# Kernel optimization log

Measured on AMD Instinct MI355X. Metric: run time of the kernel, lower is better.

The kernel has to match this reference:

```python
import jax, jax.numpy as jnp
import numpy as np
import math

B, T, N, D = 8, 12, 1000, 256
H, R = 8, 32
HD = D // H
E = 4 * D  # SwiGLU expansion


def setup_inputs() -> dict:
    key = jax.random.key(0)
    ks = jax.random.split(key, 12)
    s = 0.02
    return {
        "x": jax.random.normal(ks[0], (B, T, N, D), jnp.float32),
        "z": jax.random.normal(ks[1], (B, T, N, D), jnp.float32),
        # block params
        "norm1_w": jnp.ones((D,), jnp.float32),
        "norm2_w": jnp.ones((D,), jnp.float32),
        "alpha": jnp.float32(math.log(9)),
        "beta": jnp.float32(math.log(math.sqrt(2) + 1)),
        "gamma": jnp.float32(math.log(9)),
        "delta": jnp.float32(math.log(math.sqrt(2) + 1)),
        # low-rank attention params (Linear stored as [in, out])
        "Wq": jax.random.normal(ks[2], (D, D), jnp.float32) * s,
        "bq": jnp.zeros((D,), jnp.float32),
        "key_param": jax.random.normal(ks[3], (R, H, HD), jnp.float32),
        "Wv": jax.random.normal(ks[4], (D, D), jnp.float32) * s,
        "bv": jnp.zeros((D,), jnp.float32),
        "mha_alpha": jnp.full((H, 1), math.log(9), jnp.float32),
        "mha_beta": jnp.full((H, 1), math.log(0.01), jnp.float32),
        # SwiGLU FFN params
        "W1": jax.random.normal(ks[5], (D, E), jnp.float32) * s,
        "b1": jnp.zeros((E,), jnp.float32),
        "W2": jax.random.normal(ks[6], (D, E), jnp.float32) * s,
        "b2": jnp.zeros((E,), jnp.float32),
        "W3": jax.random.normal(ks[7], (E, D), jnp.float32) * s,
        "b3": jnp.zeros((D,), jnp.float32),
    }


def _rms_norm(x, w, eps=1e-6):
    return w * (x * jax.lax.rsqrt(jnp.mean(x * x, axis=-1, keepdims=True) + eps))


def reference(x, z, norm1_w, norm2_w, alpha, beta, gamma, delta,
              Wq, bq, key_param, Wv, bv, mha_alpha, mha_beta,
              W1, b1, W2, b2, W3, b3):
    sig = jax.nn.sigmoid
    x1 = _rms_norm(x, norm1_w)
    z1 = _rms_norm(sig(gamma) * x1 + sig(delta) * z, norm2_w)

    # SwiGLU FFN (dropout is identity in eval)
    ffn = (jax.nn.silu(x1 @ W1 + b1) * (x1 @ W2 + b2)) @ W3 + b3

    # Low-rank spatial attention
    q = (z1 @ Wq + bq).reshape(B, T, N, H, HD)
    attn = jnp.einsum('btnhd,rhd->btnhr', q, key_param) / jnp.float32(HD) ** 0.5
    xv = (x1 @ Wv + bv).reshape(B, T, N, H, HD)
    v = jnp.einsum('btnhr,btnhd->btrhd', jax.nn.softmax(attn, axis=-1), xv)
    v = jnp.einsum('btnhr,btrhd->btnhd', jax.nn.softmax(attn, axis=2), v)
    v = sig(mha_alpha) * xv + sig(mha_beta) * v  # (H,1) broadcasts over (h,d)
    mha = v.reshape(B, T, N, D)

    return sig(alpha) * ffn + sig(beta) * mha
```

## Files before the change

kernel.cpp:

```cpp
#include <hip/hip_runtime.h>
#include <math.h>

#define MT 96000
#define DD 256
#define EE 1024
#define NBT 96
#define NSEQ 1000

typedef __attribute__((ext_vector_type(8))) short bf16x8;
typedef __attribute__((ext_vector_type(4))) short bf16x4;
typedef __attribute__((ext_vector_type(4))) float f32x4;

__device__ __forceinline__ short f2b(float f) {
  union { float f; unsigned u; } v; v.f = f;
  unsigned r = (v.u + 0x7FFFu + ((v.u >> 16) & 1u)) >> 16;
  return (short)r;
}
__device__ __forceinline__ float b2f(short s) {
  union { unsigned u; float f; } v; v.u = ((unsigned)(unsigned short)s) << 16;
  return v.f;
}
__device__ __forceinline__ float sigf(float x) { return 1.f / (1.f + __expf(-x)); }
__device__ __forceinline__ f32x4 mfma16(bf16x8 a, bf16x8 b, f32x4 c) {
  return __builtin_amdgcn_mfma_f32_16x16x32_bf16(a, b, c, 0, 0, 0);
}
__device__ __forceinline__ unsigned cvtpk(float lo, float hi) {
  unsigned r;
  asm("v_cvt_pk_bf16_f32 %0, %1, %2" : "=v"(r) : "v"(lo), "v"(hi));
  return r;
}
__device__ __forceinline__ float frcp(float x) {
  float r;
  asm("v_rcp_f32 %0, %1" : "=v"(r) : "v"(x));
  return r;
}
__device__ __forceinline__ void gl_lds16(const short* gp, short* lp) {
  __builtin_amdgcn_global_load_lds(
      (const __attribute__((address_space(1))) void*)gp,
      (__attribute__((address_space(3))) void*)lp, 16, 0, 0);
}

__global__ __launch_bounds__(256) void k_prep(
    const float* __restrict__ Wq, const float* __restrict__ bq,
    const float* __restrict__ key, const float* __restrict__ Wv,
    const float* __restrict__ W1, const float* __restrict__ W2,
    const float* __restrict__ W3,
    short* __restrict__ W1t, short* __restrict__ W2t, short* __restrict__ W3t,
    short* __restrict__ Wvt, short* __restrict__ Wqkt, float* __restrict__ bqk)
{
  int i = blockIdx.x * 256 + threadIdx.x;
  { int e = i >> 8, c = i & 255;
    W1t[i] = f2b(W1[c * EE + e]);
    W2t[i] = f2b(W2[c * EE + e]); }
  { int n = i >> 10, e = i & 1023;
    W3t[i] = f2b(W3[e * DD + n]); }
  if (i < 65536) {
    int n = i >> 8, c = i & 255;
    Wvt[i] = f2b(Wv[c * DD + n]);
    int h = n >> 5, r = n & 31;
    float acc = 0.f;
    for (int d = 0; d < 32; ++d)
      acc += Wq[c * DD + h * 32 + d] * key[(r * 8 + h) * 32 + d];
    Wqkt[i] = f2b(acc * 0.17677669529663687f);
  }
  if (i < 256) {
    int h = i >> 5, r = i & 31;
    float acc = 0.f;
    for (int d = 0; d < 32; ++d)
      acc += bq[h * 32 + d] * key[(r * 8 + h) * 32 + d];
    bqk[i] = acc * 0.17677669529663687f;
  }
}

__global__ __launch_bounds__(256) void k_norm(
    const float* __restrict__ x, const float* __restrict__ z,
    const float* __restrict__ nw1, const float* __restrict__ nw2,
    const float* __restrict__ gamma, const float* __restrict__ delta,
    short* __restrict__ x1bp, short* __restrict__ z1bp)
{
  int tok = blockIdx.x * 4 + (threadIdx.x >> 6);
  int lane = threadIdx.x & 63;
  size_t rbase = (size_t)tok * DD;
  float4 xv = ((const float4*)(x + rbase))[lane];
  float ss = xv.x*xv.x + xv.y*xv.y + xv.z*xv.z + xv.w*xv.w;
  #pragma unroll
  for (int mm = 1; mm < 64; mm <<= 1) ss += __shfl_xor(ss, mm);
  float inv = rsqrtf(ss * 0.00390625f + 1e-6f);
  float4 wv = ((const float4*)nw1)[lane];
  float xa = xv.x * inv * wv.x, xb = xv.y * inv * wv.y,
        xc = xv.z * inv * wv.z, xd = xv.w * inv * wv.w;
  bf16x4 xo = { f2b(xa), f2b(xb), f2b(xc), f2b(xd) };
  ((bf16x4*)(x1bp + rbase))[lane] = xo;
  float sg = sigf(gamma[0]), sd = sigf(delta[0]);
  float4 zv = ((const float4*)(z + rbase))[lane];
  float t0 = sg*xa + sd*zv.x, t1 = sg*xb + sd*zv.y,
        t2 = sg*xc + sd*zv.z, t3 = sg*xd + sd*zv.w;
  float s2 = t0*t0 + t1*t1 + t2*t2 + t3*t3;
  #pragma unroll
  for (int mm = 1; mm < 64; mm <<= 1) s2 += __shfl_xor(s2, mm);
  float inv2 = rsqrtf(s2 * 0.00390625f + 1e-6f);
  float4 w2v = ((const float4*)nw2)[lane];
  bf16x4 zo = { f2b(t0*inv2*w2v.x), f2b(t1*inv2*w2v.y),
                f2b(t2*inv2*w2v.z), f2b(t3*inv2*w2v.w) };
  ((bf16x4*)(z1bp + rbase))[lane] = zo;
}

__global__ __launch_bounds__(256) void k_gemm_fullN(
    const short* __restrict__ A, const short* __restrict__ Bt,
    const float* __restrict__ bias, short* __restrict__ C)
{
  __shared__ __align__(16) short As[64 * 264];
  int row0 = blockIdx.x * 64;
  int tid = threadIdx.x, lane = tid & 63, w = tid >> 6;
  int l15 = lane & 15, g = lane >> 4;
  #pragma unroll
  for (int it = 0; it < 8; ++it) {
    int idx = it * 256 + tid;
    int rw = idx >> 5, ch = (idx & 31) * 8;
    *(bf16x8*)&As[rw * 264 + ch] = *(const bf16x8*)&A[(size_t)(row0 + rw) * 256 + ch];
  }
  f32x4 acc[4][4];
  #pragma unroll
  for (int tn = 0; tn < 4; ++tn) {
    float bb = bias[w * 64 + tn * 16 + l15];
    #pragma unroll
    for (int tm = 0; tm < 4; ++tm) acc[tm][tn] = (f32x4){bb, bb, bb, bb};
  }
  __syncthreads();
  #pragma unroll
  for (int kk = 0; kk < 8; ++kk) {
    bf16x8 af[4], wf[4];
    #pragma unroll
    for (int tm = 0; tm < 4; ++tm)
      af[tm] = *(const bf16x8*)&As[(tm * 16 + l15) * 264 + kk * 32 + g * 8];
    #pragma unroll
    for (int tn = 0; tn < 4; ++tn)
      wf[tn] = *(const bf16x8*)&Bt[(size_t)(w * 64 + tn * 16 + l15) * 256 + kk * 32 + g * 8];
    #pragma unroll
    for (int tn = 0; tn < 4; ++tn)
      #pragma unroll
      for (int tm = 0; tm < 4; ++tm)
        acc[tm][tn] = mfma16(af[tm], wf[tn], acc[tm][tn]);
  }
  #pragma unroll
  for (int tn = 0; tn < 4; ++tn) {
    int n = w * 64 + tn * 16 + l15;
    #pragma unroll
    for (int tm = 0; tm < 4; ++tm)
      #pragma unroll
      for (int r = 0; r < 4; ++r) {
        int m = row0 + tm * 16 + g * 4 + r;
        C[(size_t)m * 256 + n] = f2b(acc[tm][tn][r]);
      }
  }
}

__global__ __launch_bounds__(256, 2) void k_ffn(
    const short* __restrict__ x1bp,
    const short* __restrict__ W1t, const short* __restrict__ W2t,
    const short* __restrict__ W3t,
    const float* __restrict__ b1, const float* __restrict__ b2,
    const float* __restrict__ b3, const float* __restrict__ alpha,
    float* __restrict__ out)
{
  __shared__ __align__(16) short As[64 * 256];
  __shared__ __align__(16) short Hs[64 * 72];
  __shared__ __align__(16) short WR[4 * 4096];
  __shared__ __align__(16) short Bb[2048];
  int row0 = blockIdx.x * 64;
  int tid = threadIdx.x, lane = tid & 63, w = tid >> 6;
  int l15 = lane & 15, g = lane >> 4;
  int swz = l15 & 7;
  int w16 = w * 16;
  int wb = w * 4096;
  int lr = lane >> 2;
  int lc = (((lane & 3) ^ ((lane >> 3) & 3)) * 8);
  int rsw = (l15 >> 1) & 3;

  #pragma unroll
  for (int it = 0; it < 8; ++it) {
    int idx = it * 256 + tid;
    int rw = idx >> 5, c = idx & 31;
    bf16x8 v = __builtin_nontemporal_load(
        (const bf16x8*)&x1bp[(size_t)(row0 + rw) * 256 + c * 8]);
    *(bf16x8*)&As[rw * 256 + ((c ^ (rw & 7)) * 8)] = v;
  }
  {
    float4 v1 = ((const float4*)b1)[tid];
    float4 v2 = ((const float4*)b2)[tid];
    bf16x4 p1 = { f2b(v1.x), f2b(v1.y), f2b(v1.z), f2b(v1.w) };
    bf16x4 p2 = { f2b(v2.x), f2b(v2.y), f2b(v2.z), f2b(v2.w) };
    *(bf16x4*)&Bb[tid * 4] = p1;
    *(bf16x4*)&Bb[1024 + tid * 4] = p2;
  }
  f32x4 oacc[4][4];
  #pragma unroll
  for (int tn = 0; tn < 4; ++tn) {
    float bb = b3[w * 64 + tn * 16 + l15];
    #pragma unroll
    for (int tm = 0; tm < 4; ++tm) oacc[tm][tn] = (f32x4){bb, bb, bb, bb};
  }
  __syncthreads();

  #pragma unroll
  for (int s = 0; s < 4; ++s) {
    gl_lds16(W1t + (size_t)(w16 + lr) * 256 + s * 32 + lc, &WR[wb + s * 1024]);
    gl_lds16(W2t + (size_t)(w16 + lr) * 256 + s * 32 + lc, &WR[wb + s * 1024 + 512]);
  }

  for (int ec = 0; ec < 16; ++ec) {
    int e0 = ec * 64;
    int e0n = ((ec + 1) & 15) * 64;
    int ew = e0 + w16;
    bf16x4 c1b = *(const bf16x4*)&Bb[ew + g * 4];
    bf16x4 c2b = *(const bf16x4*)&Bb[1024 + ew + g * 4];
    f32x4 i1 = { b2f(c1b[0]), b2f(c1b[1]), b2f(c1b[2]), b2f(c1b[3]) };
    f32x4 i2 = { b2f(c2b[0]), b2f(c2b[1]), b2f(c2b[2]), b2f(c2b[3]) };
    f32x4 h1[4], h2[4];
    #pragma unroll
    for (int tm = 0; tm < 4; ++tm) { h1[tm] = i1; h2[tm] = i2; }
    #pragma unroll
    for (int kk = 0; kk < 8; ++kk) {
      int slot = kk & 3;
      asm volatile("s_waitcnt vmcnt(6)" ::: "memory");
      bf16x8 w1f = *(const bf16x8*)&WR[wb + slot * 1024 + l15 * 32 + ((g ^ rsw) * 8)];
      bf16x8 w2f = *(const bf16x8*)&WR[wb + slot * 1024 + 512 + l15 * 32 + ((g ^ rsw) * 8)];
      int ac = ((kk * 4 + g) ^ swz) * 8;
      bf16x8 a0 = *(const bf16x8*)&As[(l15) * 256 + ac];
      bf16x8 a1 = *(const bf16x8*)&As[(16 + l15) * 256 + ac];
      bf16x8 a2 = *(const bf16x8*)&As[(32 + l15) * 256 + ac];
      bf16x8 a3 = *(const bf16x8*)&As[(48 + l15) * 256 + ac];
      asm volatile("s_waitcnt lgkmcnt(0)" ::: "memory");
      if (kk < 4) {
        gl_lds16(W1t + (size_t)(ew + lr) * 256 + (kk + 4) * 32 + lc,
                 &WR[wb + slot * 1024]);
        gl_lds16(W2t + (size_t)(ew + lr) * 256 + (kk + 4) * 32 + lc,
                 &WR[wb + slot * 1024 + 512]);
      } else {
        int k2i = (kk - 4) >> 1, nh = kk & 1;
        const short* g3 = W3t + (size_t)(w * 64 + nh * 32 + lr) * 1024
                          + e0 + k2i * 32 + lc;
        gl_lds16(g3, &WR[wb + slot * 1024]);
        gl_lds16(g3 + 16 * 1024, &WR[wb + slot * 1024 + 512]);
      }
      h1[0] = mfma16(w1f, a0, h1[0]); h2[0] = mfma16(w2f, a0, h2[0]);
      h1[1] = mfma16(w1f, a1, h1[1]); h2[1] = mfma16(w2f, a1, h2[1]);
      h1[2] = mfma16(w1f, a2, h1[2]); h2[2] = mfma16(w2f, a2, h2[2]);
      h1[3] = mfma16(w1f, a3, h1[3]); h2[3] = mfma16(w2f, a3, h2[3]);
    }
    #pragma unroll
    for (int tm = 0; tm < 4; ++tm) {
      int m = tm * 16 + l15;
      float a0 = h1[tm][0], a1 = h1[tm][1], a2 = h1[tm][2], a3 = h1[tm][3];
      float v0 = a0 * h2[tm][0] * sigf(a0);
      float v1 = a1 * h2[tm][1] * sigf(a1);
      float v2 = a2 * h2[tm][2] * sigf(a2);
      float v3 = a3 * h2[tm][3] * sigf(a3);
      uint2 pk;
      pk.x = cvtpk(v0, v1);
      pk.y = cvtpk(v2, v3);
      *(uint2*)&Hs[m * 72 + w16 + g * 4] = pk;
    }
    asm volatile("s_waitcnt lgkmcnt(0)" ::: "memory");
    __builtin_amdgcn_sched_barrier(0);
    __builtin_amdgcn_s_barrier();
    __builtin_amdgcn_sched_barrier(0);
    #pragma unroll
    for (int k2 = 0; k2 < 2; ++k2) {
      asm volatile("s_waitcnt vmcnt(4)" ::: "memory");
      bf16x8 hf[4];
      #pragma unroll
      for (int tm = 0; tm < 4; ++tm)
        hf[tm] = *(const bf16x8*)&Hs[(tm * 16 + l15) * 72 + k2 * 32 + g * 8];
      bf16x8 w3f[4];
      #pragma unroll
      for (int tn = 0; tn < 4; ++tn)
        w3f[tn] = *(const bf16x8*)&WR[wb + (k2 * 2 + (tn >> 1)) * 1024
                                     + (tn & 1) * 512 + l15 * 32 + ((g ^ rsw) * 8)];
      asm volatile("s_waitcnt lgkmcnt(0)" ::: "memory");
      gl_lds16(W1t + (size_t)(e0n + w16 + lr) * 256 + (k2 * 2) * 32 + lc,
               &WR[wb + (k2 * 2) * 1024]);
      gl_lds16(W2t + (size_t)(e0n + w16 + lr) * 256 + (k2 * 2) * 32 + lc,
               &WR[wb + (k2 * 2) * 1024 + 512]);
      gl_lds16(W1t + (size_t)(e0n + w16 + lr) * 256 + (k2 * 2 + 1) * 32 + lc,
               &WR[wb + (k2 * 2 + 1) * 1024]);
      gl_lds16(W2t + (size_t)(e0n + w16 + lr) * 256 + (k2 * 2 + 1) * 32 + lc,
               &WR[wb + (k2 * 2 + 1) * 1024 + 512]);
      #pragma unroll
      for (int tn = 0; tn < 4; ++tn)
        #pragma unroll
        for (int tm = 0; tm < 4; ++tm)
          oacc[tm][tn] = mfma16(hf[tm], w3f[tn], oacc[tm][tn]);
    }
    __builtin_amdgcn_sched_barrier(0);
    __builtin_amdgcn_s_barrier();
    __builtin_amdgcn_sched_barrier(0);
  }
  asm volatile("s_waitcnt vmcnt(0)" ::: "memory");
  float sa = sigf(alpha[0]);
  #pragma unroll
  for (int tn = 0; tn < 4; ++tn) {
    int n = w * 64 + tn * 16 + l15;
    #pragma unroll
    for (int tm = 0; tm < 4; ++tm)
      #pragma unroll
      for (int r = 0; r < 4; ++r) {
        int m = row0 + tm * 16 + g * 4 + r;
        __builtin_nontemporal_store(sa * oacc[tm][tn][r], &out[(size_t)m * 256 + n]);
      }
  }
}

__global__ __launch_bounds__(256) void k_attn1(
    const short* __restrict__ attnb, const short* __restrict__ xvb,
    float* __restrict__ v1buf, float* __restrict__ colmax, float* __restrict__ colsum)
{
  __shared__ float xr[8][32];
  __shared__ float red[8][32][32];
  __shared__ float mred[8][32], sred[8][32];
  int gid = blockIdx.x;
  int bt = gid >> 3, h = gid & 7;
  int tid = threadIdx.x, r = tid & 31, nl = tid >> 5;
  int base = bt * NSEQ;
  float accd[32];
  #pragma unroll
  for (int d = 0; d < 32; ++d) accd[d] = 0.f;
  float mrun = -1e30f, srun = 0.f;
  for (int it = 0; it < 125; ++it) {
    int tok = base + it * 8 + nl;
    float a = b2f(attnb[(size_t)tok * 256 + h * 32 + r]);
    float rmax = a;
    #pragma unroll
    for (int mm = 16; mm > 0; mm >>= 1) rmax = fmaxf(rmax, __shfl_xor(rmax, mm));
    float ea = __expf(a - rmax);
    float rsum = ea;
    #pragma unroll
    for (int mm = 16; mm > 0; mm >>= 1) rsum += __shfl_xor(rsum, mm);
    float p1 = ea * frcp(rsum);
    float nm = fmaxf(mrun, a);
    srun = srun * __expf(mrun - nm) + __expf(a - nm);
    mrun = nm;
    xr[nl][r] = b2f(xvb[(size_t)tok * 256 + h * 32 + r]);
    #pragma unroll
    for (int d = 0; d < 32; ++d) accd[d] += p1 * xr[nl][d];
  }
  #pragma unroll
  for (int d = 0; d < 32; ++d) red[nl][r][d] = accd[d];
  mred[nl][r] = mrun; sred[nl][r] = srun;
  __syncthreads();
  for (int s = 4; s > 0; s >>= 1) {
    if (nl < s)
      #pragma unroll
      for (int d = 0; d < 32; ++d) red[nl][r][d] += red[nl + s][r][d];
    __syncthreads();
  }
  if (nl == 0) {
    for (int d = 0; d < 32; ++d) v1buf[gid * 1024 + r * 32 + d] = red[0][r][d];
    float Mv = -1e30f;
    for (int j = 0; j < 8; ++j) Mv = fmaxf(Mv, mred[j][r]);
    float Sv = 0.f;
    for (int j = 0; j < 8; ++j) Sv += sred[j][r] * __expf(mred[j][r] - Mv);
    colmax[gid * 32 + r] = Mv;
    colsum[gid * 32 + r] = Sv;
  }
}

__global__ __launch_bounds__(256) void k_attn2(
    const short* __restrict__ attnb, const short* __restrict__ xvb,
    const float* __restrict__ v1buf, const float* __restrict__ colmax,
    const float* __restrict__ colsum, const float* __restrict__ mha_alpha,
    const float* __restrict__ mha_beta, const float* __restrict__ beta,
    float* __restrict__ out)
{
  __shared__ float p2s[256];
  int bt = blockIdx.x, chunk = blockIdx.y;
  int tid = threadIdx.x;
  int h = tid >> 5, d = tid & 31;
  float v1reg[32];
  #pragma unroll
  for (int rr = 0; rr < 32; ++rr)
    v1reg[rr] = v1buf[(size_t)bt * 8192 + h * 1024 + rr * 32 + d];
  float cm  = colmax[bt * 256 + tid];
  float rcs = 1.f / colsum[bt * 256 + tid];
  float sa = sigf(mha_alpha[h]), sb = sigf(mha_beta[h]);
  float sbeta = sigf(beta[0]);
  int tok0 = bt * NSEQ + chunk * 100;
  for (int tl = 0; tl < 100; ++tl) {
    int tok = tok0 + tl;
    float a = b2f(attnb[(size_t)tok * 256 + tid]);
    p2s[tid] = __expf(a - cm) * rcs;
    float xvv = b2f(xvb[(size_t)tok * 256 + tid]);
    float v2 = 0.f;
    #pragma unroll
    for (int rr = 0; rr < 32; ++rr)
      v2 += p2s[h * 32 + rr] * v1reg[rr];
    out[(size_t)tok * 256 + tid] += sbeta * (sa * xvv + sb * v2);
  }
}

extern "C" void kernel_launch(void* const* d_in, const int* in_sizes, int n_in,
                              void* d_out, int out_size, void* d_ws, size_t ws_size,
                              hipStream_t stream) {
  const float* x        = (const float*)d_in[0];
  const float* z        = (const float*)d_in[1];
  const float* norm1_w  = (const float*)d_in[2];
  const float* norm2_w  = (const float*)d_in[3];
  const float* alpha    = (const float*)d_in[4];
  const float* beta     = (const float*)d_in[5];
  const float* gamma    = (const float*)d_in[6];
  const float* delta    = (const float*)d_in[7];
  const float* Wq       = (const float*)d_in[8];
  const float* bq       = (const float*)d_in[9];
  const float* key      = (const float*)d_in[10];
  const float* Wv       = (const float*)d_in[11];
  const float* bv       = (const float*)d_in[12];
  const float* mha_a    = (const float*)d_in[13];
  const float* mha_b    = (const float*)d_in[14];
  const float* W1       = (const float*)d_in[15];
  const float* b1       = (const float*)d_in[16];
  const float* W2       = (const float*)d_in[17];
  const float* b2       = (const float*)d_in[18];
  const float* W3       = (const float*)d_in[19];
  const float* b3       = (const float*)d_in[20];
  float* out = (float*)d_out;
  char* ws = (char*)d_ws;

  short* x1b   = (short*)(ws);
  short* z1b   = (short*)(ws + 49152000);
  short* xvb   = (short*)(ws + 98304000);
  short* attnb = (short*)(ws + 147456000);
  short* W1t   = (short*)(ws + 196608000);
  short* W2t   = (short*)(ws + 197132288);
  short* W3t   = (short*)(ws + 197656576);
  short* Wvt   = (short*)(ws + 198180864);
  short* Wqkt  = (short*)(ws + 198311936);
  float* bqk   = (float*)(ws + 198443008);
  float* v1buf = (float*)(ws + 198444032);
  float* colmax= (float*)(ws + 201589760);
  float* colsum= (float*)(ws + 201688064);

  hipLaunchKernelGGL(k_prep, dim3(1024), dim3(256), 0, stream,
                     Wq, bq, key, Wv, W1, W2, W3, W1t, W2t, W3t, Wvt, Wqkt, bqk);
  hipLaunchKernelGGL(k_norm, dim3(MT / 4), dim3(256), 0, stream,
                     x, z, norm1_w, norm2_w, gamma, delta, x1b, z1b);
  hipLaunchKernelGGL(k_gemm_fullN, dim3(MT / 64), dim3(256), 0, stream,
                     z1b, Wqkt, bqk, attnb);
  hipLaunchKernelGGL(k_gemm_fullN, dim3(MT / 64), dim3(256), 0, stream,
                     x1b, Wvt, bv, xvb);
  hipLaunchKernelGGL(k_ffn, dim3(MT / 64), dim3(256), 0, stream,
                     x1b, W1t, W2t, W3t, b1, b2, b3, alpha, out);
  hipLaunchKernelGGL(k_attn1, dim3(NBT * 8), dim3(256), 0, stream,
                     attnb, xvb, v1buf, colmax, colsum);
  hipLaunchKernelGGL(k_attn2, dim3(NBT, 10), dim3(256), 0, stream,
                     attnb, xvb, v1buf, colmax, colsum, mha_a, mha_b, beta, out);
}
```

Baseline: 726.8 us.

## Fuse RMS norms and Q/V projections into the FFN kernel

The norm kernel, both projection GEMMs and the FFN are merged into one kernel per 64-row tile. The normalized x1 and z1 tiles are computed straight into shared memory and reused for the Q·key and V projections and the FFN, so the bf16 x1/z1 intermediates are never written to or read back from global memory, and three launches are dropped. Shared memory is aliased between the z1 tile and the FFN weight ring. The cost is a longer per-block serial prologue with possible register/LDS pressure at two blocks per CU.

```diff
diff --git a/kernel.cpp b/kernel.cpp
--- a/kernel.cpp
+++ b/kernel.cpp
@@ -72,101 +72,26 @@
   }
 }
 
-__global__ __launch_bounds__(256) void k_norm(
+__global__ __launch_bounds__(256, 2) void k_fused(
     const float* __restrict__ x, const float* __restrict__ z,
     const float* __restrict__ nw1, const float* __restrict__ nw2,
     const float* __restrict__ gamma, const float* __restrict__ delta,
-    short* __restrict__ x1bp, short* __restrict__ z1bp)
-{
-  int tok = blockIdx.x * 4 + (threadIdx.x >> 6);
-  int lane = threadIdx.x & 63;
-  size_t rbase = (size_t)tok * DD;
-  float4 xv = ((const float4*)(x + rbase))[lane];
-  float ss = xv.x*xv.x + xv.y*xv.y + xv.z*xv.z + xv.w*xv.w;
-  #pragma unroll
-  for (int mm = 1; mm < 64; mm <<= 1) ss += __shfl_xor(ss, mm);
-  float inv = rsqrtf(ss * 0.00390625f + 1e-6f);
-  float4 wv = ((const float4*)nw1)[lane];
-  float xa = xv.x * inv * wv.x, xb = xv.y * inv * wv.y,
-        xc = xv.z * inv * wv.z, xd = xv.w * inv * wv.w;
-  bf16x4 xo = { f2b(xa), f2b(xb), f2b(xc), f2b(xd) };
-  ((bf16x4*)(x1bp + rbase))[lane] = xo;
-  float sg = sigf(gamma[0]), sd = sigf(delta[0]);
-  float4 zv = ((const float4*)(z + rbase))[lane];
-  float t0 = sg*xa + sd*zv.x, t1 = sg*xb + sd*zv.y,
-        t2 = sg*xc + sd*zv.z, t3 = sg*xd + sd*zv.w;
-  float s2 = t0*t0 + t1*t1 + t2*t2 + t3*t3;
-  #pragma unroll
-  for (int mm = 1; mm < 64; mm <<= 1) s2 += __shfl_xor(s2, mm);
-  float inv2 = rsqrtf(s2 * 0.00390625f + 1e-6f);
-  float4 w2v = ((const float4*)nw2)[lane];
-  bf16x4 zo = { f2b(t0*inv2*w2v.x), f2b(t1*inv2*w2v.y),
-                f2b(t2*inv2*w2v.z), f2b(t3*inv2*w2v.w) };
-  ((bf16x4*)(z1bp + rbase))[lane] = zo;
-}
-
-__global__ __launch_bounds__(256) void k_gemm_fullN(
-    const short* __restrict__ A, const short* __restrict__ Bt,
-    const float* __restrict__ bias, short* __restrict__ C)
-{
-  __shared__ __align__(16) short As[64 * 264];
-  int row0 = blockIdx.x * 64;
-  int tid = threadIdx.x, lane = tid & 63, w = tid >> 6;
-  int l15 = lane & 15, g = lane >> 4;
-  #pragma unroll
-  for (int it = 0; it < 8; ++it) {
-    int idx = it * 256 + tid;
-    int rw = idx >> 5, ch = (idx & 31) * 8;
-    *(bf16x8*)&As[rw * 264 + ch] = *(const bf16x8*)&A[(size_t)(row0 + rw) * 256 + ch];
-  }
-  f32x4 acc[4][4];
-  #pragma unroll
-  for (int tn = 0; tn < 4; ++tn) {
-    float bb = bias[w * 64 + tn * 16 + l15];
-    #pragma unroll
-    for (int tm = 0; tm < 4; ++tm) acc[tm][tn] = (f32x4){bb, bb, bb, bb};
-  }
-  __syncthreads();
-  #pragma unroll
-  for (int kk = 0; kk < 8; ++kk) {
-    bf16x8 af[4], wf[4];
-    #pragma unroll
-    for (int tm = 0; tm < 4; ++tm)
-      af[tm] = *(const bf16x8*)&As[(tm * 16 + l15) * 264 + kk * 32 + g * 8];
-    #pragma unroll
-    for (int tn = 0; tn < 4; ++tn)
-      wf[tn] = *(const bf16x8*)&Bt[(size_t)(w * 64 + tn * 16 + l15) * 256 + kk * 32 + g * 8];
-    #pragma unroll
-    for (int tn = 0; tn < 4; ++tn)
-      #pragma unroll
-      for (int tm = 0; tm < 4; ++tm)
-        acc[tm][tn] = mfma16(af[tm], wf[tn], acc[tm][tn]);
-  }
-  #pragma unroll
-  for (int tn = 0; tn < 4; ++tn) {
-    int n = w * 64 + tn * 16 + l15;
-    #pragma unroll
-    for (int tm = 0; tm < 4; ++tm)
-      #pragma unroll
-      for (int r = 0; r < 4; ++r) {
-        int m = row0 + tm * 16 + g * 4 + r;
-        C[(size_t)m * 256 + n] = f2b(acc[tm][tn][r]);
-      }
-  }
-}
-
-__global__ __launch_bounds__(256, 2) void k_ffn(
-    const short* __restrict__ x1bp,
+    const short* __restrict__ Wqkt, const float* __restrict__ bqk,
+    const short* __restrict__ Wvt, const float* __restrict__ bv,
     const short* __restrict__ W1t, const short* __restrict__ W2t,
     const short* __restrict__ W3t,
     const float* __restrict__ b1, const float* __restrict__ b2,
     const float* __restrict__ b3, const float* __restrict__ alpha,
+    short* __restrict__ attnb, short* __restrict__ xvb,
     float* __restrict__ out)
 {
-  __shared__ __align__(16) short As[64 * 256];
-  __shared__ __align__(16) short Hs[64 * 72];
-  __shared__ __align__(16) short WR[4 * 4096];
+  __shared__ __align__(16) short As[16384];
+  __shared__ __align__(16) short U[20992];
   __shared__ __align__(16) short Bb[2048];
+  short* Zs = U;
+  short* WR = U;
+  short* Hs = U + 16384;
+
   int row0 = blockIdx.x * 64;
   int tid = threadIdx.x, lane = tid & 63, w = tid >> 6;
   int l15 = lane & 15, g = lane >> 4;
@@ -177,15 +102,33 @@
   int lc = (((lane & 3) ^ ((lane >> 3) & 3)) * 8);
   int rsw = (l15 >> 1) & 3;
 
-  #pragma unroll
-  for (int it = 0; it < 8; ++it) {
-    int idx = it * 256 + tid;
-    int rw = idx >> 5, c = idx & 31;
-    bf16x8 v = __builtin_nontemporal_load(
-        (const bf16x8*)&x1bp[(size_t)(row0 + rw) * 256 + c * 8]);
-    *(bf16x8*)&As[rw * 256 + ((c ^ (rw & 7)) * 8)] = v;
-  }
   {
+    float sg = sigf(gamma[0]), sd = sigf(delta[0]);
+    float4 wv = ((const float4*)nw1)[lane];
+    float4 w2v = ((const float4*)nw2)[lane];
+    for (int t = 0; t < 16; ++t) {
+      int tl = w16 + t;
+      size_t rbase = (size_t)(row0 + tl) * 256;
+      float4 xv = ((const float4*)(x + rbase))[lane];
+      float ss = xv.x*xv.x + xv.y*xv.y + xv.z*xv.z + xv.w*xv.w;
+      #pragma unroll
+      for (int mm = 1; mm < 64; mm <<= 1) ss += __shfl_xor(ss, mm);
+      float inv = rsqrtf(ss * 0.00390625f + 1e-6f);
+      float xa = xv.x * inv * wv.x, xb = xv.y * inv * wv.y,
+            xc = xv.z * inv * wv.z, xd = xv.w * inv * wv.w;
+      bf16x4 xo = { f2b(xa), f2b(xb), f2b(xc), f2b(xd) };
+      *(bf16x4*)&As[tl * 256 + (((lane >> 1) ^ (tl & 7)) * 8) + (lane & 1) * 4] = xo;
+      float4 zv = ((const float4*)(z + rbase))[lane];
+      float t0 = sg*xa + sd*zv.x, t1 = sg*xb + sd*zv.y,
+            t2 = sg*xc + sd*zv.z, t3 = sg*xd + sd*zv.w;
+      float s2 = t0*t0 + t1*t1 + t2*t2 + t3*t3;
+      #pragma unroll
+      for (int mm = 1; mm < 64; mm <<= 1) s2 += __shfl_xor(s2, mm);
+      float inv2 = rsqrtf(s2 * 0.00390625f + 1e-6f);
+      bf16x4 zo = { f2b(t0*inv2*w2v.x), f2b(t1*inv2*w2v.y),
+                    f2b(t2*inv2*w2v.z), f2b(t3*inv2*w2v.w) };
+      *(bf16x4*)&Zs[tl * 264 + lane * 4] = zo;
+    }
     float4 v1 = ((const float4*)b1)[tid];
     float4 v2 = ((const float4*)b2)[tid];
     bf16x4 p1 = { f2b(v1.x), f2b(v1.y), f2b(v1.z), f2b(v1.w) };
@@ -193,6 +136,79 @@
     *(bf16x4*)&Bb[tid * 4] = p1;
     *(bf16x4*)&Bb[1024 + tid * 4] = p2;
   }
+  __syncthreads();
+
+  {
+    f32x4 acc[4][4];
+    #pragma unroll
+    for (int tn = 0; tn < 4; ++tn) {
+      float bb = bqk[w * 64 + tn * 16 + l15];
+      #pragma unroll
+      for (int tm = 0; tm < 4; ++tm) acc[tm][tn] = (f32x4){bb, bb, bb, bb};
+    }
+    #pragma unroll
+    for (int kk = 0; kk < 8; ++kk) {
+      bf16x8 af[4], wf[4];
+      #pragma unroll
+      for (int tm = 0; tm < 4; ++tm)
+        af[tm] = *(const bf16x8*)&Zs[(tm * 16 + l15) * 264 + kk * 32 + g * 8];
+      #pragma unroll
+      for (int tn = 0; tn < 4; ++tn)
+        wf[tn] = *(const bf16x8*)&Wqkt[(size_t)(w * 64 + tn * 16 + l15) * 256 + kk * 32 + g * 8];
+      #pragma unroll
+      for (int tn = 0; tn < 4; ++tn)
+        #pragma unroll
+        for (int tm = 0; tm < 4; ++tm)
+          acc[tm][tn] = mfma16(af[tm], wf[tn], acc[tm][tn]);
+    }
+    #pragma unroll
+    for (int tn = 0; tn < 4; ++tn) {
+      int n = w * 64 + tn * 16 + l15;
+      #pragma unroll
+      for (int tm = 0; tm < 4; ++tm)
+        #pragma unroll
+        for (int r = 0; r < 4; ++r) {
+          int m = row0 + tm * 16 + g * 4 + r;
+          attnb[(size_t)m * 256 + n] = f2b(acc[tm][tn][r]);
+        }
+    }
+  }
+  {
+    f32x4 acc[4][4];
+    #pragma unroll
+    for (int tn = 0; tn < 4; ++tn) {
+      float bb = bv[w * 64 + tn * 16 + l15];
+      #pragma unroll
+      for (int tm = 0; tm < 4; ++tm) acc[tm][tn] = (f32x4){bb, bb, bb, bb};
+    }
+    #pragma unroll
+    for (int kk = 0; kk < 8; ++kk) {
+      bf16x8 af[4], wf[4];
+      int ac = ((kk * 4 + g) ^ swz) * 8;
+      #pragma unroll
+      for (int tm = 0; tm < 4; ++tm)
+        af[tm] = *(const bf16x8*)&As[(tm * 16 + l15) * 256 + ac];
+      #pragma unroll
+      for (int tn = 0; tn < 4; ++tn)
+        wf[tn] = *(const bf16x8*)&Wvt[(size_t)(w * 64 + tn * 16 + l15) * 256 + kk * 32 + g * 8];
+      #pragma unroll
+      for (int tn = 0; tn < 4; ++tn)
+        #pragma unroll
+        for (int tm = 0; tm < 4; ++tm)
+          acc[tm][tn] = mfma16(af[tm], wf[tn], acc[tm][tn]);
+    }
+    #pragma unroll
+    for (int tn = 0; tn < 4; ++tn) {
+      int n = w * 64 + tn * 16 + l15;
+      #pragma unroll
+      for (int tm = 0; tm < 4; ++tm)
+        #pragma unroll
+        for (int r = 0; r < 4; ++r) {
+          int m = row0 + tm * 16 + g * 4 + r;
+          xvb[(size_t)m * 256 + n] = f2b(acc[tm][tn][r]);
+        }
+    }
+  }
   f32x4 oacc[4][4];
   #pragma unroll
   for (int tn = 0; tn < 4; ++tn) {
@@ -200,6 +216,9 @@
     #pragma unroll
     for (int tm = 0; tm < 4; ++tm) oacc[tm][tn] = (f32x4){bb, bb, bb, bb};
   }
+  __builtin_amdgcn_sched_barrier(0);
+  asm volatile("s_waitcnt vmcnt(0) lgkmcnt(0)" ::: "memory");
+  __builtin_amdgcn_sched_barrier(0);
   __syncthreads();
 
   #pragma unroll
@@ -425,8 +444,6 @@
   float* out = (float*)d_out;
   char* ws = (char*)d_ws;
 
-  short* x1b   = (short*)(ws);
-  short* z1b   = (short*)(ws + 49152000);
   short* xvb   = (short*)(ws + 98304000);
   short* attnb = (short*)(ws + 147456000);
   short* W1t   = (short*)(ws + 196608000);
@@ -441,14 +458,10 @@
 
   hipLaunchKernelGGL(k_prep, dim3(1024), dim3(256), 0, stream,
                      Wq, bq, key, Wv, W1, W2, W3, W1t, W2t, W3t, Wvt, Wqkt, bqk);
-  hipLaunchKernelGGL(k_norm, dim3(MT / 4), dim3(256), 0, stream,
-                     x, z, norm1_w, norm2_w, gamma, delta, x1b, z1b);
-  hipLaunchKernelGGL(k_gemm_fullN, dim3(MT / 64), dim3(256), 0, stream,
-                     z1b, Wqkt, bqk, attnb);
-  hipLaunchKernelGGL(k_gemm_fullN, dim3(MT / 64), dim3(256), 0, stream,
-                     x1b, Wvt, bv, xvb);
-  hipLaunchKernelGGL(k_ffn, dim3(MT / 64), dim3(256), 0, stream,
-                     x1b, W1t, W2t, W3t, b1, b2, b3, alpha, out);
+  hipLaunchKernelGGL(k_fused, dim3(MT / 64), dim3(256), 0, stream,
+                     x, z, norm1_w, norm2_w, gamma, delta,
+                     Wqkt, bqk, Wvt, bv, W1t, W2t, W3t,
+                     b1, b2, b3, alpha, attnb, xvb, out);
   hipLaunchKernelGGL(k_attn1, dim3(NBT * 8), dim3(256), 0, stream,
                      attnb, xvb, v1buf, colmax, colsum);
   hipLaunchKernelGGL(k_attn2, dim3(NBT, 10), dim3(256), 0, stream,
```

After: 689.9 us. 5.1% less time.
